# Kernel tuning notes

Measured on AMD Instinct MI355X. Metric: run time of the kernel, lower is better.

The kernel has to match this reference:

```python
import jax, jax.numpy as jnp
import numpy as np

B, N, K, C = 2, 2048, 48, 128
FF = 4 * C
EPS = 1e-5
SCALE = 30.0

def _gelu(x):
    return jax.nn.gelu(x, approximate=False)

def _ln(x, g, b):
    m = jnp.mean(x, axis=-1, keepdims=True)
    v = jnp.var(x, axis=-1, keepdims=True)
    return g * (x - m) * jax.lax.rsqrt(v + EPS) + b

def _gather_nodes(nodes, idx):
    # nodes [B,N,C], idx [B,N,K] -> [B,N,K,C]
    return jnp.take_along_axis(nodes[:, :, None, :], idx[..., None], axis=1)

def setup_inputs() -> dict:
    key = jax.random.key(0)
    ks = jax.random.split(key, 16)
    def w(k, i, o):
        return (jax.random.normal(k, (i, o), jnp.float32) / np.sqrt(i)).astype(jnp.float32)
    inp = {
        'h_V': jax.random.normal(ks[0], (B, N, C), jnp.float32),
        'h_E': jax.random.normal(ks[1], (B, N, K, C), jnp.float32),
        'E_idx': jax.random.randint(ks[2], (B, N, K), 0, N),
        'mask_V': jnp.ones((B, N), jnp.float32),
        'mask_attend': jnp.ones((B, N, K), jnp.float32),
        'W1_w': w(ks[3], 3 * C, C), 'W1_b': jnp.zeros((C,), jnp.float32),
        'W2_w': w(ks[4], C, C), 'W2_b': jnp.zeros((C,), jnp.float32),
        'W3_w': w(ks[5], C, C), 'W3_b': jnp.zeros((C,), jnp.float32),
        'W11_w': w(ks[6], 3 * C, C), 'W11_b': jnp.zeros((C,), jnp.float32),
        'W12_w': w(ks[7], C, C), 'W12_b': jnp.zeros((C,), jnp.float32),
        'W13_w': w(ks[8], C, C), 'W13_b': jnp.zeros((C,), jnp.float32),
        'Win_w': w(ks[9], C, FF), 'Win_b': jnp.zeros((FF,), jnp.float32),
        'Wout_w': w(ks[10], FF, C), 'Wout_b': jnp.zeros((C,), jnp.float32),
        'g1': jnp.ones((C,), jnp.float32), 'b1': jnp.zeros((C,), jnp.float32),
        'g2': jnp.ones((C,), jnp.float32), 'b2': jnp.zeros((C,), jnp.float32),
        'g3': jnp.ones((C,), jnp.float32), 'b3': jnp.zeros((C,), jnp.float32),
    }
    return inp

def _edge_mlp(h_V, h_E, E_idx, Wa_w, Wa_b, Wb_w, Wb_b, Wc_w, Wc_b):
    h_nbr = _gather_nodes(h_V, E_idx)                       # [B,N,K,C]
    h_ctr = jnp.broadcast_to(h_V[:, :, None, :], h_nbr.shape)
    h_EV = jnp.concatenate([h_ctr, h_E, h_nbr], axis=-1)   # [B,N,K,3C]
    h = _gelu(h_EV @ Wa_w + Wa_b)
    h = _gelu(h @ Wb_w + Wb_b)
    return h @ Wc_w + Wc_b                                  # [B,N,K,C]

def reference(h_V, h_E, E_idx, mask_V, mask_attend,
              W1_w, W1_b, W2_w, W2_b, W3_w, W3_b,
              W11_w, W11_b, W12_w, W12_b, W13_w, W13_b,
              Win_w, Win_b, Wout_w, Wout_b,
              g1, b1, g2, b2, g3, b3):
    # message pass on nodes
    h_msg = _edge_mlp(h_V, h_E, E_idx, W1_w, W1_b, W2_w, W2_b, W3_w, W3_b)
    h_msg = mask_attend[..., None] * h_msg
    dh = jnp.sum(h_msg, axis=-2) / SCALE
    h_V = _ln(h_V + dh, g1, b1)
    # position-wise FFN
    dh = _gelu(h_V @ Win_w + Win_b) @ Wout_w + Wout_b
    h_V = _ln(h_V + dh, g2, b2)
    h_V = mask_V[..., None] * h_V
    # edge update
    h_msg = _edge_mlp(h_V, h_E, E_idx, W11_w, W11_b, W12_w, W12_b, W13_w, W13_b)
    h_E = _ln(h_E + h_msg, g3, b3)
    return (h_V, h_E)
```

## Files before the change

kernel.cpp:

```cpp
#include <hip/hip_runtime.h>
#include <hip/hip_bf16.h>

#define BB 2
#define NN 2048
#define KE 48
#define CC 128
#define FFD 512
#define K3 384

typedef short sx8 __attribute__((ext_vector_type(8)));
typedef float fx4 __attribute__((ext_vector_type(4)));

__device__ __forceinline__ short f2bs(float f) {
    __bf16 h = (__bf16)f;
    return __builtin_bit_cast(short, h);
}

__device__ __forceinline__ float gelu_f(float x) {
    float z = fabsf(x) * 0.70710678118654752f;
    float e = __expf(-z * z);
    float t = __builtin_amdgcn_rcpf(fmaf(0.3275911f, z, 1.0f));
    float poly = t * fmaf(t, fmaf(t, fmaf(t, fmaf(t, 1.061405429f, -1.453152027f),
                                          1.421413741f), -0.284496736f), 0.254829592f);
    float erf = 1.0f - poly * e;
    float phi = fmaf(copysignf(erf, x), 0.5f, 0.5f);
    return x * phi;
}

__device__ __forceinline__ sx8 cvt8f(const float* p) {
    float4 a = *(const float4*)p;
    float4 b = *(const float4*)(p + 4);
    sx8 r;
    r[0] = f2bs(a.x); r[1] = f2bs(a.y); r[2] = f2bs(a.z); r[3] = f2bs(a.w);
    r[4] = f2bs(b.x); r[5] = f2bs(b.y); r[6] = f2bs(b.z); r[7] = f2bs(b.w);
    return r;
}

__device__ __forceinline__ sx8 pack8(float4 a, float4 b) {
    sx8 r;
    r[0] = f2bs(a.x); r[1] = f2bs(a.y); r[2] = f2bs(a.z); r[3] = f2bs(a.w);
    r[4] = f2bs(b.x); r[5] = f2bs(b.y); r[6] = f2bs(b.z); r[7] = f2bs(b.w);
    return r;
}

__global__ void prep_weights(const float* __restrict__ W1, const float* __restrict__ W2,
                             const float* __restrict__ W3, const float* __restrict__ W11,
                             const float* __restrict__ W12, const float* __restrict__ W13,
                             const float* __restrict__ Win, const float* __restrict__ Wout,
                             short* __restrict__ wt) {
    int i = blockIdx.x * 256 + threadIdx.x;
    const float* src;
    short* dst;
    int R, S, local;
    if (i < 49152)       { src = W1;   dst = wt;          R = 384; S = 128; local = i; }
    else if (i < 65536)  { src = W2;   dst = wt + 49152;  R = 128; S = 128; local = i - 49152; }
    else if (i < 81920)  { src = W3;   dst = wt + 65536;  R = 128; S = 128; local = i - 65536; }
    else if (i < 131072) { src = W11;  dst = wt + 81920;  R = 384; S = 128; local = i - 81920; }
    else if (i < 147456) { src = W12;  dst = wt + 131072; R = 128; S = 128; local = i - 131072; }
    else if (i < 163840) { src = W13;  dst = wt + 147456; R = 128; S = 128; local = i - 147456; }
    else if (i < 229376) { src = Win;  dst = wt + 163840; R = 128; S = 512; local = i - 163840; }
    else                 { src = Wout; dst = wt + 229376; R = 512; S = 128; local = i - 229376; }
    int c = local / R;
    int r = local - c * R;
    dst[local] = f2bs(src[r * S + c]);
}

__global__ __launch_bounds__(256) void precompute_P(
    const float* __restrict__ hv, const short* __restrict__ WT,
    const float* __restrict__ bias, float* __restrict__ Pc,
    float* __restrict__ Pn) {
    __shared__ __align__(16) short Abf[16 * 136];
    const int tid = threadIdx.x;
    const int bn  = blockIdx.x;
    const int wave = tid >> 6, lane = tid & 63, q = lane >> 4, m16 = lane & 15;
    const int col0 = wave * 32 + m16, col1 = col0 + 16;

    {
        int row = tid >> 4, seg = tid & 15;
        Abf[row * 136 + seg * 8 + 0] = 0;
        *(sx8*)(Abf + row * 136 + seg * 8) = cvt8f(hv + (size_t)(bn * 16 + row) * CC + seg * 8);
    }
    __syncthreads();

    fx4 c0, c1, n0, n1;
#pragma unroll
    for (int r = 0; r < 4; ++r) { c0[r] = 0.f; c1[r] = 0.f; n0[r] = 0.f; n1[r] = 0.f; }
#pragma unroll
    for (int kk = 0; kk < 4; ++kk) {
        sx8 af = *(const sx8*)(Abf + m16 * 136 + kk * 32 + q * 8);
        sx8 bc0 = *(const sx8*)(WT + col0 * K3 + kk * 32 + q * 8);
        sx8 bc1 = *(const sx8*)(WT + col1 * K3 + kk * 32 + q * 8);
        sx8 bn0 = *(const sx8*)(WT + col0 * K3 + 256 + kk * 32 + q * 8);
        sx8 bn1 = *(const sx8*)(WT + col1 * K3 + 256 + kk * 32 + q * 8);
        c0 = __builtin_amdgcn_mfma_f32_16x16x32_bf16(af, bc0, c0, 0, 0, 0);
        c1 = __builtin_amdgcn_mfma_f32_16x16x32_bf16(af, bc1, c1, 0, 0, 0);
        n0 = __builtin_amdgcn_mfma_f32_16x16x32_bf16(af, bn0, n0, 0, 0, 0);
        n1 = __builtin_amdgcn_mfma_f32_16x16x32_bf16(af, bn1, n1, 0, 0, 0);
    }
    float bi0 = bias[col0], bi1 = bias[col1];
#pragma unroll
    for (int r = 0; r < 4; ++r) {
        int node = bn * 16 + q * 4 + r;
        Pc[(size_t)node * CC + col0] = c0[r] + bi0;
        Pc[(size_t)node * CC + col1] = c1[r] + bi1;
        Pn[(size_t)node * CC + col0] = n0[r];
        Pn[(size_t)node * CC + col1] = n1[r];
    }
}

template <int PASS>
__global__ __launch_bounds__(256, 5) void edge_pass(
    const float* __restrict__ hVsrc, const float* __restrict__ hE,
    const int* __restrict__ Eidx,
    const short* __restrict__ WaT,
    const short* __restrict__ WbT, const float* __restrict__ Wbb,
    const short* __restrict__ WcT, const float* __restrict__ Wcb,
    const float* __restrict__ Pc, const float* __restrict__ Pn,
    const float* __restrict__ mask_att, float* __restrict__ hv1_out,
    const float* __restrict__ gamma, const float* __restrict__ beta,
    float* __restrict__ hE_out) {
    __shared__ __align__(16) unsigned char smem_raw[PASS == 1 ? 15120 : 25344];

    short* A0   = (short*)smem_raw;
    short* Xs   = (short*)smem_raw;
    float* S    = (float*)smem_raw;
    float* dhp  = (float*)(smem_raw + 13056);
    float* redp = (float*)(smem_raw + 15104);

    const int tid = threadIdx.x;
    const int bn  = blockIdx.x;
    const int bb  = bn >> 11;
    const int wave = tid >> 6, lane = tid & 63, q = lane >> 4, m16 = lane & 15;
    const int col0 = wave * 32 + m16;
    const int col1 = col0 + 16;
    const int r0 = tid >> 4, seg = tid & 15;

    int e[3][4];
#pragma unroll
    for (int mt = 0; mt < 3; ++mt)
#pragma unroll
        for (int r = 0; r < 4; ++r)
            e[mt][r] = Eidx[bn * KE + mt * 16 + q * 4 + r];

    float pc0 = Pc[(size_t)bn * CC + col0];
    float pc1 = Pc[(size_t)bn * CC + col1];
    float pn0[3][4], pn1[3][4];
#pragma unroll
    for (int mt = 0; mt < 3; ++mt)
#pragma unroll
        for (int r = 0; r < 4; ++r) {
            size_t prow = ((size_t)bb * NN + e[mt][r]) * CC;
            pn0[mt][r] = Pn[prow + col0];
            pn1[mt][r] = Pn[prow + col1];
        }

    {
        const float* he = hE + (size_t)bn * KE * CC + seg * 8;
        float4 h0a = *(const float4*)(he + r0 * CC);
        float4 h0b = *(const float4*)(he + r0 * CC + 4);
        float4 h1a = *(const float4*)(he + (r0 + 16) * CC);
        float4 h1b = *(const float4*)(he + (r0 + 16) * CC + 4);
        float4 h2a = *(const float4*)(he + (r0 + 32) * CC);
        float4 h2b = *(const float4*)(he + (r0 + 32) * CC + 4);
        *(sx8*)(A0 + r0 * 136 + seg * 8)        = pack8(h0a, h0b);
        *(sx8*)(A0 + (r0 + 16) * 136 + seg * 8) = pack8(h1a, h1b);
        *(sx8*)(A0 + (r0 + 32) * 136 + seg * 8) = pack8(h2a, h2b);
    }

    sx8 b0[4], b1[4];
#pragma unroll
    for (int kk = 0; kk < 4; ++kk) {
        b0[kk] = *(const sx8*)(WaT + col0 * K3 + 128 + kk * 32 + q * 8);
        b1[kk] = *(const sx8*)(WaT + col1 * K3 + 128 + kk * 32 + q * 8);
    }
    __syncthreads();

    fx4 acc[3][2];
#pragma unroll
    for (int mt = 0; mt < 3; ++mt)
#pragma unroll
        for (int nt = 0; nt < 2; ++nt)
#pragma unroll
            for (int r = 0; r < 4; ++r) acc[mt][nt][r] = 0.0f;
#pragma unroll
    for (int kk = 0; kk < 4; ++kk) {
#pragma unroll
        for (int mt = 0; mt < 3; ++mt) {
            sx8 af = *(const sx8*)(A0 + (mt * 16 + m16) * 136 + kk * 32 + q * 8);
            acc[mt][0] = __builtin_amdgcn_mfma_f32_16x16x32_bf16(af, b0[kk], acc[mt][0], 0, 0, 0);
            acc[mt][1] = __builtin_amdgcn_mfma_f32_16x16x32_bf16(af, b1[kk], acc[mt][1], 0, 0, 0);
        }
    }

    sx8 p0[4], p1[4];
#pragma unroll
    for (int kk = 0; kk < 4; ++kk) {
        p0[kk] = *(const sx8*)(WbT + col0 * CC + kk * 32 + q * 8);
        p1[kk] = *(const sx8*)(WbT + col1 * CC + kk * 32 + q * 8);
    }
    __syncthreads();

#pragma unroll
    for (int mt = 0; mt < 3; ++mt)
#pragma unroll
        for (int r = 0; r < 4; ++r) {
            int row = mt * 16 + q * 4 + r;
            Xs[row * 136 + col0] = f2bs(gelu_f(acc[mt][0][r] + pc0 + pn0[mt][r]));
            Xs[row * 136 + col1] = f2bs(gelu_f(acc[mt][1][r] + pc1 + pn1[mt][r]));
        }
    __syncthreads();

    fx4 acc2[3][2];
#pragma unroll
    for (int mt = 0; mt < 3; ++mt)
#pragma unroll
        for (int nt = 0; nt < 2; ++nt)
#pragma unroll
            for (int r = 0; r < 4; ++r) acc2[mt][nt][r] = 0.0f;
#pragma unroll
    for (int kk = 0; kk < 4; ++kk) {
#pragma unroll
        for (int mt = 0; mt < 3; ++mt) {
            sx8 af = *(const sx8*)(Xs + (mt * 16 + m16) * 136 + kk * 32 + q * 8);
            acc2[mt][0] = __builtin_amdgcn_mfma_f32_16x16x32_bf16(af, p0[kk], acc2[mt][0], 0, 0, 0);
            acc2[mt][1] = __builtin_amdgcn_mfma_f32_16x16x32_bf16(af, p1[kk], acc2[mt][1], 0, 0, 0);
        }
    }

    sx8 t0[4], t1[4];
#pragma unroll
    for (int kk = 0; kk < 4; ++kk) {
        t0[kk] = *(const sx8*)(WcT + col0 * CC + kk * 32 + q * 8);
        t1[kk] = *(const sx8*)(WcT + col1 * CC + kk * 32 + q * 8);
    }
    float mrow[12];
    float res0[12], res1[12];
    if constexpr (PASS == 1) {
#pragma unroll
        for (int mt = 0; mt < 3; ++mt)
#pragma unroll
            for (int r = 0; r < 4; ++r)
                mrow[mt * 4 + r] = mask_att[bn * KE + mt * 16 + q * 4 + r];
    } else {
#pragma unroll
        for (int mt = 0; mt < 3; ++mt)
#pragma unroll
            for (int r = 0; r < 4; ++r) {
                int row = mt * 16 + q * 4 + r;
                res0[mt * 4 + r] = hE[((size_t)bn * KE + row) * CC + col0];
                res1[mt * 4 + r] = hE[((size_t)bn * KE + row) * CC + col1];
            }
    }
    __syncthreads();

    {
        float bb0 = Wbb[col0], bb1 = Wbb[col1];
#pragma unroll
        for (int mt = 0; mt < 3; ++mt)
#pragma unroll
            for (int r = 0; r < 4; ++r) {
                int row = mt * 16 + q * 4 + r;
                Xs[row * 136 + col0] = f2bs(gelu_f(acc2[mt][0][r] + bb0));
                Xs[row * 136 + col1] = f2bs(gelu_f(acc2[mt][1][r] + bb1));
            }
    }
    __syncthreads();

    fx4 acc3[3][2];
#pragma unroll
    for (int mt = 0; mt < 3; ++mt)
#pragma unroll
        for (int nt = 0; nt < 2; ++nt)
#pragma unroll
            for (int r = 0; r < 4; ++r) acc3[mt][nt][r] = 0.0f;
#pragma unroll
    for (int kk = 0; kk < 4; ++kk) {
#pragma unroll
        for (int mt = 0; mt < 3; ++mt) {
            sx8 af = *(const sx8*)(Xs + (mt * 16 + m16) * 136 + kk * 32 + q * 8);
            acc3[mt][0] = __builtin_amdgcn_mfma_f32_16x16x32_bf16(af, t0[kk], acc3[mt][0], 0, 0, 0);
            acc3[mt][1] = __builtin_amdgcn_mfma_f32_16x16x32_bf16(af, t1[kk], acc3[mt][1], 0, 0, 0);
        }
    }

    float bc0 = Wcb[col0], bc1 = Wcb[col1];

    if constexpr (PASS == 1) {
        float ps0 = 0.f, ps1 = 0.f;
#pragma unroll
        for (int mt = 0; mt < 3; ++mt)
#pragma unroll
            for (int r = 0; r < 4; ++r) {
                float m = mrow[mt * 4 + r];
                ps0 += m * (acc3[mt][0][r] + bc0);
                ps1 += m * (acc3[mt][1][r] + bc1);
            }
        dhp[q * 128 + col0] = ps0;
        dhp[q * 128 + col1] = ps1;
        __syncthreads();
        float val = 0.f;
        if (tid < 128) {
            float dh = dhp[tid] + dhp[128 + tid] + dhp[256 + tid] + dhp[384 + tid];
            val = hVsrc[(size_t)bn * CC + tid] + dh * (1.0f / 30.0f);
            float sv1 = val, sv2 = val * val;
#pragma unroll
            for (int m = 32; m >= 1; m >>= 1) {
                sv1 += __shfl_xor(sv1, m);
                sv2 += __shfl_xor(sv2, m);
            }
            if ((tid & 63) == 0) {
                redp[(tid >> 6) * 2]     = sv1;
                redp[(tid >> 6) * 2 + 1] = sv2;
            }
        }
        __syncthreads();
        if (tid < 128) {
            float mean = (redp[0] + redp[2]) * (1.0f / 128.0f);
            float var  = (redp[1] + redp[3]) * (1.0f / 128.0f) - mean * mean;
            float rstd = rsqrtf(fmaxf(var, 0.0f) + 1e-5f);
            hv1_out[(size_t)bn * CC + tid] = gamma[tid] * (val - mean) * rstd + beta[tid];
        }
    } else {
        __syncthreads();
#pragma unroll
        for (int mt = 0; mt < 3; ++mt)
#pragma unroll
            for (int r = 0; r < 4; ++r) {
                int row = mt * 16 + q * 4 + r;
                S[row * 132 + col0] = res0[mt * 4 + r] + acc3[mt][0][r] + bc0;
                S[row * 132 + col1] = res1[mt * 4 + r] + acc3[mt][1][r] + bc1;
            }
        __syncthreads();
        int g = tid >> 5, l32 = tid & 31;
        for (int r = g; r < 48; r += 8) {
            float x0 = S[r * 132 + l32];
            float x1 = S[r * 132 + l32 + 32];
            float x2 = S[r * 132 + l32 + 64];
            float x3 = S[r * 132 + l32 + 96];
            float sv1 = x0 + x1 + x2 + x3;
            float sv2 = x0 * x0 + x1 * x1 + x2 * x2 + x3 * x3;
#pragma unroll
            for (int m = 16; m >= 1; m >>= 1) {
                sv1 += __shfl_xor(sv1, m, 32);
                sv2 += __shfl_xor(sv2, m, 32);
            }
            float mean = sv1 * (1.0f / 128.0f);
            float var  = sv2 * (1.0f / 128.0f) - mean * mean;
            float rstd = rsqrtf(fmaxf(var, 0.0f) + 1e-5f);
            float* orow = hE_out + ((size_t)bn * KE + r) * CC;
            orow[l32]      = gamma[l32] * (x0 - mean) * rstd + beta[l32];
            orow[l32 + 32] = gamma[l32 + 32] * (x1 - mean) * rstd + beta[l32 + 32];
            orow[l32 + 64] = gamma[l32 + 64] * (x2 - mean) * rstd + beta[l32 + 64];
            orow[l32 + 96] = gamma[l32 + 96] * (x3 - mean) * rstd + beta[l32 + 96];
        }
    }
}

__global__ __launch_bounds__(256, 1) void ffn_kernel(
    float* __restrict__ hv, const short* __restrict__ WinT,
    const float* __restrict__ Winb, const short* __restrict__ WoutT,
    const float* __restrict__ Woutb, const float* __restrict__ g2,
    const float* __restrict__ b2, const float* __restrict__ maskV) {
    __shared__ __align__(16) float hvF[16 * 132];
    __shared__ __align__(16) short Abf[16 * 136];
    __shared__ __align__(16) short Xs[16 * 520];

    const int tid = threadIdx.x;
    const int bn  = blockIdx.x;
    const int wave = tid >> 6, lane = tid & 63, q = lane >> 4, m16 = lane & 15;
    const int col0 = wave * 32 + m16, col1 = col0 + 16;

    sx8 bw[4][8];
#pragma unroll
    for (int kk = 0; kk < 4; ++kk)
#pragma unroll
        for (int nt = 0; nt < 8; ++nt)
            bw[kk][nt] = *(const sx8*)(WinT + (wave * 128 + nt * 16 + m16) * CC + kk * 32 + q * 8);

    for (int i = tid; i < 512; i += 256) {
        int row = i >> 5;
        int c4  = (i & 31) * 4;
        float4 v = *(const float4*)(hv + (bn * 16 + row) * CC + c4);
        hvF[row * 132 + c4]     = v.x;
        hvF[row * 132 + c4 + 1] = v.y;
        hvF[row * 132 + c4 + 2] = v.z;
        hvF[row * 132 + c4 + 3] = v.w;
        Abf[row * 136 + c4]     = f2bs(v.x);
        Abf[row * 136 + c4 + 1] = f2bs(v.y);
        Abf[row * 136 + c4 + 2] = f2bs(v.z);
        Abf[row * 136 + c4 + 3] = f2bs(v.w);
    }
    __syncthreads();

    fx4 acc1[8];
#pragma unroll
    for (int nt = 0; nt < 8; ++nt)
#pragma unroll
        for (int r = 0; r < 4; ++r) acc1[nt][r] = 0.0f;

#pragma unroll
    for (int kk = 0; kk < 4; ++kk) {
        sx8 af = *(const sx8*)(Abf + m16 * 136 + kk * 32 + q * 8);
#pragma unroll
        for (int nt = 0; nt < 8; ++nt)
            acc1[nt] = __builtin_amdgcn_mfma_f32_16x16x32_bf16(af, bw[kk][nt], acc1[nt], 0, 0, 0);
    }

    sx8 c0a[16], c1a[16];
#pragma unroll
    for (int kk = 0; kk < 16; ++kk) {
        c0a[kk] = *(const sx8*)(WoutT + col0 * FFD + kk * 32 + q * 8);
        c1a[kk] = *(const sx8*)(WoutT + col1 * FFD + kk * 32 + q * 8);
    }

#pragma unroll
    for (int nt = 0; nt < 8; ++nt) {
        int coln = wave * 128 + nt * 16 + m16;
        float bi = Winb[coln];
#pragma unroll
        for (int r = 0; r < 4; ++r) {
            int row = q * 4 + r;
            Xs[row * 520 + coln] = f2bs(gelu_f(acc1[nt][r] + bi));
        }
    }
    __syncthreads();

    fx4 o0, o1;
#pragma unroll
    for (int r = 0; r < 4; ++r) { o0[r] = 0.0f; o1[r] = 0.0f; }
#pragma unroll
    for (int kk = 0; kk < 16; ++kk) {
        sx8 af = *(const sx8*)(Xs + m16 * 520 + kk * 32 + q * 8);
        o0 = __builtin_amdgcn_mfma_f32_16x16x32_bf16(af, c0a[kk], o0, 0, 0, 0);
        o1 = __builtin_amdgcn_mfma_f32_16x16x32_bf16(af, c1a[kk], o1, 0, 0, 0);
    }
    {
        float bo0 = Woutb[col0], bo1 = Woutb[col1];
#pragma unroll
        for (int r = 0; r < 4; ++r) {
            int row = q * 4 + r;
            hvF[row * 132 + col0] += o0[r] + bo0;
            hvF[row * 132 + col1] += o1[r] + bo1;
        }
    }
    __syncthreads();

    int g = tid >> 5, l32 = tid & 31;
#pragma unroll
    for (int rr = 0; rr < 2; ++rr) {
        int row = g + rr * 8;
        float x0 = hvF[row * 132 + l32];
        float x1 = hvF[row * 132 + l32 + 32];
        float x2 = hvF[row * 132 + l32 + 64];
        float x3 = hvF[row * 132 + l32 + 96];
        float s1 = x0 + x1 + x2 + x3;
        float s2 = x0 * x0 + x1 * x1 + x2 * x2 + x3 * x3;
#pragma unroll
        for (int m = 16; m >= 1; m >>= 1) {
            s1 += __shfl_xor(s1, m, 32);
            s2 += __shfl_xor(s2, m, 32);
        }
        float mean = s1 * (1.0f / 128.0f);
        float var  = s2 * (1.0f / 128.0f) - mean * mean;
        float rstd = rsqrtf(fmaxf(var, 0.0f) + 1e-5f);
        int node = bn * 16 + row;
        float mk = maskV[node];
        float* orow = hv + node * CC;
        orow[l32]      = mk * (g2[l32] * (x0 - mean) * rstd + b2[l32]);
        orow[l32 + 32] = mk * (g2[l32 + 32] * (x1 - mean) * rstd + b2[l32 + 32]);
        orow[l32 + 64] = mk * (g2[l32 + 64] * (x2 - mean) * rstd + b2[l32 + 64]);
        orow[l32 + 96] = mk * (g2[l32 + 96] * (x3 - mean) * rstd + b2[l32 + 96]);
    }
}

extern "C" void kernel_launch(void* const* d_in, const int* in_sizes, int n_in,
                              void* d_out, int out_size, void* d_ws, size_t ws_size,
                              hipStream_t stream) {
    (void)in_sizes; (void)n_in; (void)out_size; (void)ws_size;
    const float* hV    = (const float*)d_in[0];
    const float* hE    = (const float*)d_in[1];
    const int*   Eidx  = (const int*)d_in[2];
    const float* maskV = (const float*)d_in[3];
    const float* maskA = (const float*)d_in[4];
    const float* W1w  = (const float*)d_in[5];
    const float* W1b  = (const float*)d_in[6];
    const float* W2w  = (const float*)d_in[7];
    const float* W2b  = (const float*)d_in[8];
    const float* W3w  = (const float*)d_in[9];
    const float* W3b  = (const float*)d_in[10];
    const float* W11w = (const float*)d_in[11];
    const float* W11b = (const float*)d_in[12];
    const float* W12w = (const float*)d_in[13];
    const float* W12b = (const float*)d_in[14];
    const float* W13w = (const float*)d_in[15];
    const float* W13b = (const float*)d_in[16];
    const float* Winw = (const float*)d_in[17];
    const float* Winb = (const float*)d_in[18];
    const float* Woutw = (const float*)d_in[19];
    const float* Woutb = (const float*)d_in[20];
    const float* g1 = (const float*)d_in[21];
    const float* b1 = (const float*)d_in[22];
    const float* g2 = (const float*)d_in[23];
    const float* b2 = (const float*)d_in[24];
    const float* g3 = (const float*)d_in[25];
    const float* b3 = (const float*)d_in[26];

    short* wt   = (short*)d_ws;
    float* Pc   = (float*)((char*)d_ws + 589824);
    float* Pn   = Pc + (size_t)BB * NN * CC;
    float* outV = (float*)d_out;
    float* outE = outV + (size_t)BB * NN * CC;

    prep_weights<<<1152, 256, 0, stream>>>(W1w, W2w, W3w, W11w, W12w, W13w, Winw, Woutw, wt);
    precompute_P<<<256, 256, 0, stream>>>(hV, wt, W1b, Pc, Pn);
    edge_pass<1><<<BB * NN, 256, 0, stream>>>(hV, hE, Eidx,
                                              wt, wt + 49152, W2b, wt + 65536, W3b,
                                              Pc, Pn, maskA, outV, g1, b1, nullptr);
    ffn_kernel<<<256, 256, 0, stream>>>(outV, wt + 163840, Winb, wt + 229376, Woutb, g2, b2, maskV);
    precompute_P<<<256, 256, 0, stream>>>(outV, wt + 81920, W11b, Pc, Pn);
    edge_pass<2><<<BB * NN, 256, 0, stream>>>(outV, hE, Eidx,
                                              wt + 81920, wt + 131072, W12b, wt + 147456, W13b,
                                              Pc, Pn, nullptr, nullptr, g3, b3, outE);
}
```

Before: 348.9 us.

## Fuse second P precompute into FFN kernel and double-buffer edge smem

The second precompute_P launch is folded into the FFN kernel's epilogue. The normalized hV rows are staged as bf16 in shared memory there and the center/neighbor projections are computed with MFMA in the same kernel, removing one launch and one re-read of hV. In edge_pass, the intermediate activations now ping-pong between two shared buffers (A0 and X1), which lets two __syncthreads barriers be dropped. The cost is a larger fixed shared-memory footprint for PASS 1, which may reduce occupancy, and a redundant zero store in precompute_P is also removed.

Result: faster. 339.0 us (-2.9%).

```diff
diff --git a/kernel.cpp b/kernel.cpp
--- a/kernel.cpp
+++ b/kernel.cpp
@@ -77,7 +77,6 @@
 
     {
         int row = tid >> 4, seg = tid & 15;
-        Abf[row * 136 + seg * 8 + 0] = 0;
         *(sx8*)(Abf + row * 136 + seg * 8) = cvt8f(hv + (size_t)(bn * 16 + row) * CC + seg * 8);
     }
     __syncthreads();
@@ -119,13 +118,12 @@
     const float* __restrict__ mask_att, float* __restrict__ hv1_out,
     const float* __restrict__ gamma, const float* __restrict__ beta,
     float* __restrict__ hE_out) {
-    __shared__ __align__(16) unsigned char smem_raw[PASS == 1 ? 15120 : 25344];
-
+    __shared__ __align__(16) unsigned char smem_raw[26112];
     short* A0   = (short*)smem_raw;
-    short* Xs   = (short*)smem_raw;
+    short* X1   = (short*)(smem_raw + 13056);
     float* S    = (float*)smem_raw;
     float* dhp  = (float*)(smem_raw + 13056);
-    float* redp = (float*)(smem_raw + 15104);
+    float* redp = (float*)(smem_raw + 13056 + 2048);
 
     const int tid = threadIdx.x;
     const int bn  = blockIdx.x;
@@ -198,15 +196,14 @@
         p0[kk] = *(const sx8*)(WbT + col0 * CC + kk * 32 + q * 8);
         p1[kk] = *(const sx8*)(WbT + col1 * CC + kk * 32 + q * 8);
     }
-    __syncthreads();
 
 #pragma unroll
     for (int mt = 0; mt < 3; ++mt)
 #pragma unroll
         for (int r = 0; r < 4; ++r) {
             int row = mt * 16 + q * 4 + r;
-            Xs[row * 136 + col0] = f2bs(gelu_f(acc[mt][0][r] + pc0 + pn0[mt][r]));
-            Xs[row * 136 + col1] = f2bs(gelu_f(acc[mt][1][r] + pc1 + pn1[mt][r]));
+            X1[row * 136 + col0] = f2bs(gelu_f(acc[mt][0][r] + pc0 + pn0[mt][r]));
+            X1[row * 136 + col1] = f2bs(gelu_f(acc[mt][1][r] + pc1 + pn1[mt][r]));
         }
     __syncthreads();
 
@@ -221,7 +218,7 @@
     for (int kk = 0; kk < 4; ++kk) {
 #pragma unroll
         for (int mt = 0; mt < 3; ++mt) {
-            sx8 af = *(const sx8*)(Xs + (mt * 16 + m16) * 136 + kk * 32 + q * 8);
+            sx8 af = *(const sx8*)(X1 + (mt * 16 + m16) * 136 + kk * 32 + q * 8);
             acc2[mt][0] = __builtin_amdgcn_mfma_f32_16x16x32_bf16(af, p0[kk], acc2[mt][0], 0, 0, 0);
             acc2[mt][1] = __builtin_amdgcn_mfma_f32_16x16x32_bf16(af, p1[kk], acc2[mt][1], 0, 0, 0);
         }
@@ -251,7 +248,6 @@
                 res1[mt * 4 + r] = hE[((size_t)bn * KE + row) * CC + col1];
             }
     }
-    __syncthreads();
 
     {
         float bb0 = Wbb[col0], bb1 = Wbb[col1];
@@ -260,8 +256,8 @@
 #pragma unroll
             for (int r = 0; r < 4; ++r) {
                 int row = mt * 16 + q * 4 + r;
-                Xs[row * 136 + col0] = f2bs(gelu_f(acc2[mt][0][r] + bb0));
-                Xs[row * 136 + col1] = f2bs(gelu_f(acc2[mt][1][r] + bb1));
+                A0[row * 136 + col0] = f2bs(gelu_f(acc2[mt][0][r] + bb0));
+                A0[row * 136 + col1] = f2bs(gelu_f(acc2[mt][1][r] + bb1));
             }
     }
     __syncthreads();
@@ -277,7 +273,7 @@
     for (int kk = 0; kk < 4; ++kk) {
 #pragma unroll
         for (int mt = 0; mt < 3; ++mt) {
-            sx8 af = *(const sx8*)(Xs + (mt * 16 + m16) * 136 + kk * 32 + q * 8);
+            sx8 af = *(const sx8*)(A0 + (mt * 16 + m16) * 136 + kk * 32 + q * 8);
             acc3[mt][0] = __builtin_amdgcn_mfma_f32_16x16x32_bf16(af, t0[kk], acc3[mt][0], 0, 0, 0);
             acc3[mt][1] = __builtin_amdgcn_mfma_f32_16x16x32_bf16(af, t1[kk], acc3[mt][1], 0, 0, 0);
         }
@@ -360,7 +356,9 @@
     float* __restrict__ hv, const short* __restrict__ WinT,
     const float* __restrict__ Winb, const short* __restrict__ WoutT,
     const float* __restrict__ Woutb, const float* __restrict__ g2,
-    const float* __restrict__ b2, const float* __restrict__ maskV) {
+    const float* __restrict__ b2, const float* __restrict__ maskV,
+    const short* __restrict__ W11T, const float* __restrict__ b11,
+    float* __restrict__ Pc, float* __restrict__ Pn) {
     __shared__ __align__(16) float hvF[16 * 132];
     __shared__ __align__(16) short Abf[16 * 136];
     __shared__ __align__(16) short Xs[16 * 520];
@@ -466,10 +464,46 @@
         int node = bn * 16 + row;
         float mk = maskV[node];
         float* orow = hv + node * CC;
-        orow[l32]      = mk * (g2[l32] * (x0 - mean) * rstd + b2[l32]);
-        orow[l32 + 32] = mk * (g2[l32 + 32] * (x1 - mean) * rstd + b2[l32 + 32]);
-        orow[l32 + 64] = mk * (g2[l32 + 64] * (x2 - mean) * rstd + b2[l32 + 64]);
-        orow[l32 + 96] = mk * (g2[l32 + 96] * (x3 - mean) * rstd + b2[l32 + 96]);
+        float y0 = mk * (g2[l32] * (x0 - mean) * rstd + b2[l32]);
+        float y1 = mk * (g2[l32 + 32] * (x1 - mean) * rstd + b2[l32 + 32]);
+        float y2 = mk * (g2[l32 + 64] * (x2 - mean) * rstd + b2[l32 + 64]);
+        float y3 = mk * (g2[l32 + 96] * (x3 - mean) * rstd + b2[l32 + 96]);
+        orow[l32]      = y0;
+        orow[l32 + 32] = y1;
+        orow[l32 + 64] = y2;
+        orow[l32 + 96] = y3;
+        Abf[row * 136 + l32]      = f2bs(y0);
+        Abf[row * 136 + l32 + 32] = f2bs(y1);
+        Abf[row * 136 + l32 + 64] = f2bs(y2);
+        Abf[row * 136 + l32 + 96] = f2bs(y3);
+    }
+    __syncthreads();
+
+    {
+        fx4 pc0a, pc1a, pn0a, pn1a;
+#pragma unroll
+        for (int r = 0; r < 4; ++r) { pc0a[r] = 0.f; pc1a[r] = 0.f; pn0a[r] = 0.f; pn1a[r] = 0.f; }
+#pragma unroll
+        for (int kk = 0; kk < 4; ++kk) {
+            sx8 af = *(const sx8*)(Abf + m16 * 136 + kk * 32 + q * 8);
+            sx8 bc0 = *(const sx8*)(W11T + col0 * K3 + kk * 32 + q * 8);
+            sx8 bc1 = *(const sx8*)(W11T + col1 * K3 + kk * 32 + q * 8);
+            sx8 bn0 = *(const sx8*)(W11T + col0 * K3 + 256 + kk * 32 + q * 8);
+            sx8 bn1 = *(const sx8*)(W11T + col1 * K3 + 256 + kk * 32 + q * 8);
+            pc0a = __builtin_amdgcn_mfma_f32_16x16x32_bf16(af, bc0, pc0a, 0, 0, 0);
+            pc1a = __builtin_amdgcn_mfma_f32_16x16x32_bf16(af, bc1, pc1a, 0, 0, 0);
+            pn0a = __builtin_amdgcn_mfma_f32_16x16x32_bf16(af, bn0, pn0a, 0, 0, 0);
+            pn1a = __builtin_amdgcn_mfma_f32_16x16x32_bf16(af, bn1, pn1a, 0, 0, 0);
+        }
+        float bi0 = b11[col0], bi1 = b11[col1];
+#pragma unroll
+        for (int r = 0; r < 4; ++r) {
+            int node = bn * 16 + q * 4 + r;
+            Pc[(size_t)node * CC + col0] = pc0a[r] + bi0;
+            Pc[(size_t)node * CC + col1] = pc1a[r] + bi1;
+            Pn[(size_t)node * CC + col0] = pn0a[r];
+            Pn[(size_t)node * CC + col1] = pn1a[r];
+        }
     }
 }
 
@@ -516,8 +550,8 @@
     edge_pass<1><<<BB * NN, 256, 0, stream>>>(hV, hE, Eidx,
                                               wt, wt + 49152, W2b, wt + 65536, W3b,
                                               Pc, Pn, maskA, outV, g1, b1, nullptr);
-    ffn_kernel<<<256, 256, 0, stream>>>(outV, wt + 163840, Winb, wt + 229376, Woutb, g2, b2, maskV);
-    precompute_P<<<256, 256, 0, stream>>>(outV, wt + 81920, W11b, Pc, Pn);
+    ffn_kernel<<<256, 256, 0, stream>>>(outV, wt + 163840, Winb, wt + 229376, Woutb, g2, b2, maskV,
+                                        wt + 81920, W11b, Pc, Pn);
     edge_pass<2><<<BB * NN, 256, 0, stream>>>(outV, hE, Eidx,
                                               wt + 81920, wt + 131072, W12b, wt + 147456, W13b,
                                               Pc, Pn, nullptr, nullptr, g3, b3, outE);
```
